# Optimization experiments

Measured on AMD Instinct MI355X. Metric: run time of the kernel, lower is better.

Reference implementation:

```python
import jax, jax.numpy as jnp
import numpy as np

B, C, H, W = 4, 32, 64, 64
D_STATE, D_CONV = 16, 4


def _mamba(x, Win, convw, convb, Wx, Wdt, dtb, Alog, D, Wout, dt_rank):
    Bsz, L, _ = x.shape
    d_in, K = convw.shape
    xz = x @ Win.T                                  # (B, L, 2*d_inner)
    xc, z = xz[..., :d_in], xz[..., d_in:]
    xp = jnp.pad(xc, ((0, 0), (K - 1, 0), (0, 0)))  # causal left pad
    xconv = convb + sum(convw[:, k] * xp[:, k:k + L, :] for k in range(K))
    xa = jax.nn.silu(xconv)                         # (B, L, d_inner)
    xdbl = xa @ Wx.T                                # (B, L, dt_rank + 2*N)
    dt = jax.nn.softplus(xdbl[..., :dt_rank] @ Wdt.T + dtb)     # (B, L, d_inner)
    Bm = xdbl[..., dt_rank:dt_rank + D_STATE]                   # (B, L, N)
    Cm = xdbl[..., dt_rank + D_STATE:]                          # (B, L, N)
    A = -jnp.exp(Alog)                                          # (d_inner, N)
    dA = jnp.exp(dt[..., None] * A)                             # (B, L, d_inner, N)
    dBu = dt[..., None] * Bm[:, :, None, :] * xa[..., None]     # (B, L, d_inner, N)

    def step(h, inp):
        dA_t, dBu_t, C_t = inp
        h = dA_t * h + dBu_t
        return h, jnp.einsum('bdn,bn->bd', h, C_t)

    h0 = jnp.zeros((Bsz, d_in, D_STATE), x.dtype)
    _, ys = jax.lax.scan(step, h0, (dA.transpose(1, 0, 2, 3), dBu.transpose(1, 0, 2, 3), Cm.transpose(1, 0, 2)))
    y = ys.transpose(1, 0, 2) + D * xa
    return (y * jax.nn.silu(z)) @ Wout.T


def _line_seqs(x):
    # x: (B,C,H,W) -> four (B, H*W, C) directional scan orders
    hf = x.reshape(B, C, H * W).transpose(0, 2, 1)
    hb = hf[:, ::-1, :]
    wf = x.transpose(0, 1, 3, 2).reshape(B, C, H * W).transpose(0, 2, 1)
    wb = wf[:, ::-1, :]
    return hf, hb, wf, wb


def _oss(fo1, fo2, p1, p2):
    hf, hb, wf, wb = _line_seqs(fo1)
    fop = jnp.concatenate([hf, hb, wf, wb], axis=2)       # (B, HW, 4C)
    fop = _mamba(fop, *p1, dt_rank=8)
    fop = fop.reshape(B, H * W, 4, C).sum(2)              # (B, HW, C)
    fop = fop.transpose(0, 2, 1).reshape(B, C, H, W)
    residual = fop * fo2
    foc = residual.mean(axis=(2, 3)).reshape(B, C, 1)     # adaptive_avg_pool2d (1,1)
    foc = jnp.concatenate([foc, foc[:, ::-1, :]], axis=2) # (B, C, 2)
    foc = _mamba(foc, *p2, dt_rank=1)
    foc = foc.sum(2, keepdims=True)[..., None]            # (B, C, 1, 1)
    return foc * residual + residual


def setup_inputs() -> dict:
    key = jax.random.key(0)
    ks = jax.random.split(key, 18)
    def n(k, shape, s=0.02):
        return jax.random.normal(k, shape, jnp.float32) * s
    dm1, di1, dr1 = 4 * C, 8 * C, 8
    dm2, di2, dr2 = 2, 4, 1
    return {
        'fo1': jax.random.normal(ks[0], (B, C, H, W), jnp.float32),
        'fo2': jax.random.normal(ks[1], (B, C, H, W), jnp.float32),
        'm1_Win': n(ks[2], (2 * di1, dm1)),
        'm1_convw': n(ks[3], (di1, D_CONV), 0.2),
        'm1_convb': n(ks[4], (di1,), 0.1),
        'm1_Wx': n(ks[5], (dr1 + 2 * D_STATE, di1)),
        'm1_Wdt': n(ks[6], (di1, dr1), 0.1),
        'm1_dtb': n(ks[7], (di1,), 0.5),
        'm1_Alog': jnp.log(jnp.tile(jnp.arange(1, D_STATE + 1, dtype=jnp.float32), (di1, 1))),
        'm1_D': jnp.ones((di1,), jnp.float32),
        'm1_Wout': n(ks[8], (dm1, di1)),
        'm2_Win': n(ks[9], (2 * di2, dm2)),
        'm2_convw': n(ks[10], (di2, D_CONV), 0.2),
        'm2_convb': n(ks[11], (di2,), 0.1),
        'm2_Wx': n(ks[12], (dr2 + 2 * D_STATE, di2)),
        'm2_Wdt': n(ks[13], (di2, dr2), 0.1),
        'm2_dtb': n(ks[14], (di2,), 0.5),
        'm2_Alog': jnp.log(jnp.tile(jnp.arange(1, D_STATE + 1, dtype=jnp.float32), (di2, 1))),
        'm2_D': jnp.ones((di2,), jnp.float32),
        'm2_Wout': n(ks[15], (dm2, di2)),
    }


def reference(fo1, fo2, m1_Win, m1_convw, m1_convb, m1_Wx, m1_Wdt, m1_dtb, m1_Alog, m1_D, m1_Wout,
              m2_Win, m2_convw, m2_convb, m2_Wx, m2_Wdt, m2_dtb, m2_Alog, m2_D, m2_Wout):
    p1 = (m1_Win, m1_convw, m1_convb, m1_Wx, m1_Wdt, m1_dtb, m1_Alog, m1_D, m1_Wout)
    p2 = (m2_Win, m2_convw, m2_convb, m2_Wx, m2_Wdt, m2_dtb, m2_Alog, m2_D, m2_Wout)
    return _oss(fo1, fo2, p1, p2)
```

## Files before the change

### kernel.cpp

```cpp
#include <hip/hip_runtime.h>
#include <cstddef>


typedef __attribute__((ext_vector_type(8))) short short8v;
typedef __attribute__((ext_vector_type(4))) float f32x4;

__device__ __forceinline__ float siluf(float x) { return x / (1.f + __expf(-x)); }
__device__ __forceinline__ float softplusf(float x) { return (x > 20.f) ? x : log1pf(__expf(x)); }
__device__ __forceinline__ unsigned short f2bf(float f) {
  union { float f; unsigned int u; } v; v.f = f;
  unsigned int r = v.u + 0x7fff + ((v.u >> 16) & 1);
  return (unsigned short)(r >> 16);
}

__global__ __launch_bounds__(256) void k_build_fop(const float* __restrict__ fo1,
                                                   unsigned short* __restrict__ fopb) {
  int idx = blockIdx.x * 256 + threadIdx.x;
  int j = idx & 127;
  int l = (idx >> 7) & 4095;
  int b = idx >> 19;
  int g = j >> 5, c = j & 31;
  const float* base = fo1 + (size_t)(b * 32 + c) * 4096;
  int li;
  if (g == 0)      li = l;
  else if (g == 1) li = 4095 - l;
  else if (g == 2) li = ((l & 63) << 6) + (l >> 6);
  else { int i2 = 4095 - l; li = ((i2 & 63) << 6) + (i2 >> 6); }
  fopb[idx] = f2bf(base[li]);
}

__global__ __launch_bounds__(256) void k_gemm1_mfma(const unsigned short* __restrict__ A,
                                                    const float* __restrict__ Win,
                                                    float* __restrict__ C) {
  __shared__ unsigned short As[128][136];
  __shared__ unsigned short Bs[64][136];
  int t = threadIdx.x;
  int bm = blockIdx.x * 128, bn = blockIdx.y * 64;
#pragma unroll
  for (int it = 0; it < 8; ++it) {
    int idx = t + it * 256;
    int r = idx >> 4, kc = idx & 15;
    short8v v = *(const short8v*)&A[(size_t)(bm + r) * 128 + kc * 8];
    *(short8v*)&As[r][kc * 8] = v;
  }
#pragma unroll
  for (int it = 0; it < 8; ++it) {
    int idx = t + it * 256;
    int r = idx >> 5, kq = idx & 31;
    float4 w = *(const float4*)&Win[(size_t)(bn + r) * 128 + kq * 4];
    ushort4 h;
    h.x = f2bf(w.x); h.y = f2bf(w.y); h.z = f2bf(w.z); h.w = f2bf(w.w);
    *(ushort4*)&Bs[r][kq * 4] = h;
  }
  __syncthreads();
  int lane = t & 63, w = t >> 6;
  int wm = (w & 1) * 64, wn = (w >> 1) * 32;
  int lr = lane & 15, lg = lane >> 4;
  f32x4 acc[4][2] = {};
#pragma unroll
  for (int k0 = 0; k0 < 128; k0 += 32) {
    short8v a[4], b[2];
#pragma unroll
    for (int mf = 0; mf < 4; ++mf)
      a[mf] = *(const short8v*)&As[wm + mf * 16 + lr][k0 + lg * 8];
#pragma unroll
    for (int nf = 0; nf < 2; ++nf)
      b[nf] = *(const short8v*)&Bs[wn + nf * 16 + lr][k0 + lg * 8];
#pragma unroll
    for (int mf = 0; mf < 4; ++mf)
#pragma unroll
      for (int nf = 0; nf < 2; ++nf)
        acc[mf][nf] = __builtin_amdgcn_mfma_f32_16x16x32_bf16(a[mf], b[nf], acc[mf][nf], 0, 0, 0);
  }
#pragma unroll
  for (int mf = 0; mf < 4; ++mf)
#pragma unroll
    for (int nf = 0; nf < 2; ++nf)
#pragma unroll
      for (int r = 0; r < 4; ++r) {
        size_t row = bm + wm + mf * 16 + lg * 4 + r;
        C[row * 512 + bn + wn + nf * 16 + lr] = acc[mf][nf][r];
      }
}

__global__ __launch_bounds__(256) void k_gemm_nt(const float* __restrict__ A,
                                                 const float* __restrict__ W,
                                                 float* __restrict__ C,
                                                 int M, int N, int K, int lda) {
  __shared__ float As[32][68];
  __shared__ float Ws[32][68];
  int tid = threadIdx.x;
  int bm = blockIdx.x * 64;
  int bn = blockIdx.y * 64;
  int tx = tid & 15, ty = tid >> 4;
  float acc[4][4] = {};
  for (int k0 = 0; k0 < K; k0 += 32) {
#pragma unroll
    for (int it = 0; it < 2; ++it) {
      int idx = tid + it * 256;
      int r = idx >> 3;
      int kq = idx & 7;
      float4 v = *(const float4*)&A[(size_t)(bm + r) * lda + k0 + kq * 4];
      As[kq * 4 + 0][r] = v.x; As[kq * 4 + 1][r] = v.y;
      As[kq * 4 + 2][r] = v.z; As[kq * 4 + 3][r] = v.w;
      int n = bn + r;
      float4 w = make_float4(0.f, 0.f, 0.f, 0.f);
      if (n < N) w = *(const float4*)&W[(size_t)n * K + k0 + kq * 4];
      Ws[kq * 4 + 0][r] = w.x; Ws[kq * 4 + 1][r] = w.y;
      Ws[kq * 4 + 2][r] = w.z; Ws[kq * 4 + 3][r] = w.w;
    }
    __syncthreads();
#pragma unroll
    for (int k = 0; k < 32; ++k) {
      float4 a = *(const float4*)&As[k][ty * 4];
      float4 w = *(const float4*)&Ws[k][tx * 4];
      float av[4] = {a.x, a.y, a.z, a.w};
      float wv[4] = {w.x, w.y, w.z, w.w};
#pragma unroll
      for (int i = 0; i < 4; ++i)
#pragma unroll
        for (int j = 0; j < 4; ++j)
          acc[i][j] = fmaf(av[i], wv[j], acc[i][j]);
    }
    __syncthreads();
  }
#pragma unroll
  for (int i = 0; i < 4; ++i) {
    size_t m = bm + ty * 4 + i;
#pragma unroll
    for (int j = 0; j < 4; ++j) {
      int n = bn + tx * 4 + j;
      if (n < N) C[m * N + n] = acc[i][j];
    }
  }
}

__global__ __launch_bounds__(256) void k_conv_silu(const float* __restrict__ xz,
                                                   const float* __restrict__ convw,
                                                   const float* __restrict__ convb,
                                                   float* __restrict__ xa) {
  int row = blockIdx.x;
  int l = row & 4095;
  int d = threadIdx.x;
  float4 w = *(const float4*)&convw[d * 4];
  float acc = convb[d];
  const float* p = xz + (size_t)row * 512 + d;
  if (l >= 3) acc = fmaf(w.x, p[-3 * 512], acc);
  if (l >= 2) acc = fmaf(w.y, p[-2 * 512], acc);
  if (l >= 1) acc = fmaf(w.z, p[-1 * 512], acc);
  acc = fmaf(w.w, p[0], acc);
  xa[(size_t)row * 256 + d] = siluf(acc);
}

__global__ __launch_bounds__(256) void k_scan_p1(const float* __restrict__ xa,
                                                 const float* __restrict__ xdbl,
                                                 const float* __restrict__ Wdt,
                                                 const float* __restrict__ dtb,
                                                 const float* __restrict__ Alog,
                                                 float* __restrict__ Pb,
                                                 float* __restrict__ Qb) {
  __shared__ f32x4 xrow[32][10];
  __shared__ float xas[32][256];
  int t = threadIdx.x;
  int blk = blockIdx.x;
  int ch = blk & 127, b = blk >> 7;
  size_t row0 = (size_t)b * 4096 + ch * 32;
  for (int i = t; i < 320; i += 256) {
    int s = i / 10, q = i - s * 10;
    xrow[s][q] = *(const f32x4*)&xdbl[(row0 + s) * 40 + q * 4];
  }
#pragma unroll
  for (int it = 0; it < 8; ++it) {
    int i = t + it * 256;
    int s = i >> 6, q = i & 63;
    *(f32x4*)&xas[s][q * 4] = *(const f32x4*)&xa[(row0 + s) * 256 + q * 4];
  }
  __syncthreads();
  int d = t;
  f32x4 w0 = *(const f32x4*)&Wdt[d * 8];
  f32x4 w1 = *(const f32x4*)&Wdt[d * 8 + 4];
  float bias = dtb[d];
  float A[16], P[16], Q[16];
#pragma unroll
  for (int g = 0; g < 4; ++g) {
    f32x4 al = *(const f32x4*)&Alog[d * 16 + g * 4];
#pragma unroll
    for (int j = 0; j < 4; ++j) {
      A[g * 4 + j] = -__expf(al[j]);
      P[g * 4 + j] = 1.f;
      Q[g * 4 + j] = 0.f;
    }
  }
#pragma unroll 2
  for (int s = 0; s < 32; ++s) {
    f32x4 x0 = xrow[s][0], x1 = xrow[s][1];
    float v = bias;
#pragma unroll
    for (int j = 0; j < 4; ++j) v = fmaf(x0[j], w0[j], v);
#pragma unroll
    for (int j = 0; j < 4; ++j) v = fmaf(x1[j], w1[j], v);
    float ex = __expf(v);
    float dtv = (v > 20.f) ? v : __logf(1.f + ex);
    float du = dtv * xas[s][d];
    f32x4 bm[4];
#pragma unroll
    for (int g = 0; g < 4; ++g) bm[g] = xrow[s][2 + g];
#pragma unroll
    for (int n = 0; n < 16; ++n) {
      float e = __expf(dtv * A[n]);
      Q[n] = fmaf(e, Q[n], du * bm[n >> 2][n & 3]);
      P[n] *= e;
    }
  }
  size_t ob = (size_t)ch * 16384 + b * 4096 + d * 16;
#pragma unroll
  for (int g = 0; g < 4; ++g) {
    *(f32x4*)&Pb[ob + g * 4] = *(f32x4*)&P[g * 4];
    *(f32x4*)&Qb[ob + g * 4] = *(f32x4*)&Q[g * 4];
  }
}

__global__ __launch_bounds__(256) void k_scan_p2(const float* __restrict__ Pb,
                                                 const float* __restrict__ Qb,
                                                 float* __restrict__ Hin) {
  int t = blockIdx.x * 256 + threadIdx.x;
  float h = 0.f;
  size_t o = t;
#pragma unroll 8
  for (int ch = 0; ch < 128; ++ch) {
    Hin[o] = h;
    h = fmaf(Pb[o], h, Qb[o]);
    o += 16384;
  }
}

__global__ __launch_bounds__(256) void k_scan_p3(const float* __restrict__ xa,
                                                 const float* __restrict__ xdbl,
                                                 const float* __restrict__ Wdt,
                                                 const float* __restrict__ dtb,
                                                 const float* __restrict__ Alog,
                                                 const float* __restrict__ Hin,
                                                 const float* __restrict__ Dp,
                                                 const float* __restrict__ xz,
                                                 float* __restrict__ ym) {
  __shared__ f32x4 xrow[32][10];
  __shared__ float xas[32][256];
  int t = threadIdx.x;
  int blk = blockIdx.x;
  int ch = blk & 127, b = blk >> 7;
  size_t row0 = (size_t)b * 4096 + ch * 32;
  for (int i = t; i < 320; i += 256) {
    int s = i / 10, q = i - s * 10;
    xrow[s][q] = *(const f32x4*)&xdbl[(row0 + s) * 40 + q * 4];
  }
#pragma unroll
  for (int it = 0; it < 8; ++it) {
    int i = t + it * 256;
    int s = i >> 6, q = i & 63;
    *(f32x4*)&xas[s][q * 4] = *(const f32x4*)&xa[(row0 + s) * 256 + q * 4];
  }
  __syncthreads();
  int d = t;
  f32x4 w0 = *(const f32x4*)&Wdt[d * 8];
  f32x4 w1 = *(const f32x4*)&Wdt[d * 8 + 4];
  float bias = dtb[d];
  float Dd = Dp[d];
  float A[16], h[16];
  size_t hb = (size_t)ch * 16384 + b * 4096 + d * 16;
#pragma unroll
  for (int g = 0; g < 4; ++g) {
    f32x4 al = *(const f32x4*)&Alog[d * 16 + g * 4];
    f32x4 hv = *(const f32x4*)&Hin[hb + g * 4];
#pragma unroll
    for (int j = 0; j < 4; ++j) {
      A[g * 4 + j] = -__expf(al[j]);
      h[g * 4 + j] = hv[j];
    }
  }
  const float* zp = xz + row0 * 512 + 256 + d;
  float* yo = ym + row0 * 256 + d;
#pragma unroll 2
  for (int s = 0; s < 32; ++s) {
    f32x4 x0 = xrow[s][0], x1 = xrow[s][1];
    float v = bias;
#pragma unroll
    for (int j = 0; j < 4; ++j) v = fmaf(x0[j], w0[j], v);
#pragma unroll
    for (int j = 0; j < 4; ++j) v = fmaf(x1[j], w1[j], v);
    float ex = __expf(v);
    float dtv = (v > 20.f) ? v : __logf(1.f + ex);
    float xav = xas[s][d];
    float du = dtv * xav;
    f32x4 bm[4], cm[4];
#pragma unroll
    for (int g = 0; g < 4; ++g) { bm[g] = xrow[s][2 + g]; cm[g] = xrow[s][6 + g]; }
    float y0 = 0.f, y1 = 0.f, y2 = 0.f, y3 = 0.f;
#pragma unroll
    for (int n = 0; n < 16; n += 4) {
      float e0 = __expf(dtv * A[n]);
      float e1 = __expf(dtv * A[n + 1]);
      float e2 = __expf(dtv * A[n + 2]);
      float e3 = __expf(dtv * A[n + 3]);
      f32x4 bv = bm[n >> 2], cv = cm[n >> 2];
      h[n]     = fmaf(e0, h[n],     du * bv[0]);
      h[n + 1] = fmaf(e1, h[n + 1], du * bv[1]);
      h[n + 2] = fmaf(e2, h[n + 2], du * bv[2]);
      h[n + 3] = fmaf(e3, h[n + 3], du * bv[3]);
      y0 = fmaf(h[n], cv[0], y0);
      y1 = fmaf(h[n + 1], cv[1], y1);
      y2 = fmaf(h[n + 2], cv[2], y2);
      y3 = fmaf(h[n + 3], cv[3], y3);
    }
    float y = (y0 + y1) + (y2 + y3) + Dd * xav;
    float z = zp[s * 512];
    yo[s * 256] = y * siluf(z);
  }
}

__global__ __launch_bounds__(256) void k_gemm3(const float* __restrict__ A,
                                               const float* __restrict__ Wout,
                                               float* __restrict__ CT) {
  __shared__ float As[32][68];
  __shared__ float Ws[32][68];
  int tid = threadIdx.x;
  int bm = blockIdx.x * 64;
  int tx = tid & 15, ty = tid >> 4;
  float acc[4][4] = {};
  for (int k0 = 0; k0 < 256; k0 += 32) {
#pragma unroll
    for (int it = 0; it < 2; ++it) {
      int idx = tid + it * 256;
      int r = idx >> 3;
      int kq = idx & 7;
      float4 v = *(const float4*)&A[(size_t)(bm + r) * 256 + k0 + kq * 4];
      As[kq * 4 + 0][r] = v.x; As[kq * 4 + 1][r] = v.y;
      As[kq * 4 + 2][r] = v.z; As[kq * 4 + 3][r] = v.w;
      float4 w = make_float4(0.f, 0.f, 0.f, 0.f);
      if (r < 32) {
#pragma unroll
        for (int g = 0; g < 4; ++g) {
          float4 wg = *(const float4*)&Wout[(size_t)(r + g * 32) * 256 + k0 + kq * 4];
          w.x += wg.x; w.y += wg.y; w.z += wg.z; w.w += wg.w;
        }
      }
      Ws[kq * 4 + 0][r] = w.x; Ws[kq * 4 + 1][r] = w.y;
      Ws[kq * 4 + 2][r] = w.z; Ws[kq * 4 + 3][r] = w.w;
    }
    __syncthreads();
#pragma unroll
    for (int k = 0; k < 32; ++k) {
      float4 a = *(const float4*)&As[k][ty * 4];
      float4 w = *(const float4*)&Ws[k][tx * 4];
      float av[4] = {a.x, a.y, a.z, a.w};
      float wv[4] = {w.x, w.y, w.z, w.w};
#pragma unroll
      for (int i = 0; i < 4; ++i)
#pragma unroll
        for (int j = 0; j < 4; ++j)
          acc[i][j] = fmaf(av[i], wv[j], acc[i][j]);
    }
    __syncthreads();
  }
#pragma unroll
  for (int j = 0; j < 4; ++j) {
    int n = tx * 4 + j;
    if (n < 32) {
      float4 v = make_float4(acc[0][j], acc[1][j], acc[2][j], acc[3][j]);
      *(float4*)&CT[(size_t)n * 16384 + bm + ty * 4] = v;
    }
  }
}

__global__ __launch_bounds__(256) void k_res_foc(const float* __restrict__ CT,
                                                 const float* __restrict__ fo2,
                                                 float* __restrict__ res,
                                                 float* __restrict__ foc) {
  int bc = blockIdx.x;
  int b = bc >> 5, c = bc & 31;
  int t = threadIdx.x;
  const float* src = CT + (size_t)c * 16384 + (size_t)b * 4096;
  const float* f2 = fo2 + (size_t)bc * 4096;
  float* rp = res + (size_t)bc * 4096;
  float s = 0.f;
  for (int i = t * 4; i < 4096; i += 1024) {
    float4 a = *(const float4*)&src[i];
    float4 f = *(const float4*)&f2[i];
    float4 r = make_float4(a.x * f.x, a.y * f.y, a.z * f.z, a.w * f.w);
    *(float4*)&rp[i] = r;
    s += r.x + r.y + r.z + r.w;
  }
  __shared__ float red[256];
  red[t] = s;
  __syncthreads();
  for (int off = 128; off > 0; off >>= 1) {
    if (t < off) red[t] += red[t + off];
    __syncthreads();
  }
  if (t == 0) foc[bc] = red[0] * (1.f / 4096.f);
}

__global__ __launch_bounds__(256) void k_mamba2(const float* __restrict__ foc,
                                                const float* __restrict__ Win2,
                                                const float* __restrict__ convw2,
                                                const float* __restrict__ convb2,
                                                const float* __restrict__ Wx2,
                                                const float* __restrict__ Wdt2,
                                                const float* __restrict__ dtb2,
                                                const float* __restrict__ Alog2,
                                                const float* __restrict__ D2,
                                                const float* __restrict__ Wout2,
                                                float* __restrict__ scale) {
  __shared__ float foc_s[128];
  __shared__ float xz2_s[4][32][8];
  __shared__ float xa2_s[4][32][4];
  __shared__ float xdbl2_s[4][32][33];
  __shared__ float dt2_s[4][32][4];
  __shared__ float ym2_s[4][32][4];
  int t = threadIdx.x;
  if (t < 128) foc_s[t] = foc[t];
  __syncthreads();
  for (int i = t; i < 1024; i += 256) {
    int j = i & 7, l = (i >> 3) & 31, b = i >> 8;
    float x0 = foc_s[b * 32 + l], x1 = foc_s[b * 32 + 31 - l];
    xz2_s[b][l][j] = x0 * Win2[j * 2] + x1 * Win2[j * 2 + 1];
  }
  __syncthreads();
  for (int i = t; i < 512; i += 256) {
    int d = i & 3, l = (i >> 2) & 31, b = i >> 7;
    float acc = convb2[d];
#pragma unroll
    for (int k = 0; k < 4; ++k) {
      int ls = l + k - 3;
      if (ls >= 0) acc = fmaf(convw2[d * 4 + k], xz2_s[b][ls][d], acc);
    }
    xa2_s[b][l][d] = siluf(acc);
  }
  __syncthreads();
  for (int i = t; i < 4224; i += 256) {
    int r = i % 33, l = (i / 33) & 31, b = i / 1056;
    float s = 0.f;
#pragma unroll
    for (int d = 0; d < 4; ++d) s = fmaf(xa2_s[b][l][d], Wx2[r * 4 + d], s);
    xdbl2_s[b][l][r] = s;
  }
  __syncthreads();
  for (int i = t; i < 512; i += 256) {
    int d = i & 3, l = (i >> 2) & 31, b = i >> 7;
    float s = xdbl2_s[b][l][0] * Wdt2[d] + dtb2[d];
    dt2_s[b][l][d] = softplusf(s);
  }
  __syncthreads();
  {
    int n = t & 15, d = (t >> 4) & 3, b = t >> 6;
    float A = -__expf(Alog2[d * 16 + n]);
    float h = 0.f;
    for (int l = 0; l < 32; ++l) {
      float dtv = dt2_s[b][l][d];
      float xav = xa2_s[b][l][d];
      float e = __expf(dtv * A);
      h = fmaf(e, h, dtv * xdbl2_s[b][l][1 + n] * xav);
      float yp = h * xdbl2_s[b][l][17 + n];
      yp += __shfl_xor(yp, 1);
      yp += __shfl_xor(yp, 2);
      yp += __shfl_xor(yp, 4);
      yp += __shfl_xor(yp, 8);
      if (n == 0) {
        float z = xz2_s[b][l][4 + d];
        float y = yp + D2[d] * xav;
        ym2_s[b][l][d] = y * siluf(z);
      }
    }
  }
  __syncthreads();
  if (t < 128) {
    int l = t & 31, b = t >> 5;
    float s = 0.f;
#pragma unroll
    for (int d = 0; d < 4; ++d) s = fmaf(ym2_s[b][l][d], Wout2[d] + Wout2[4 + d], s);
    scale[t] = s;
  }
}

__global__ __launch_bounds__(256) void k_final(const float* __restrict__ res,
                                               const float* __restrict__ scale,
                                               float* __restrict__ out) {
  int idx = blockIdx.x * 256 + threadIdx.x;
  out[idx] = res[idx] * (1.f + scale[idx >> 12]);
}

extern "C" void kernel_launch(void* const* d_in, const int* in_sizes, int n_in,
                              void* d_out, int out_size, void* d_ws, size_t ws_size,
                              hipStream_t stream) {
  const float* fo1    = (const float*)d_in[0];
  const float* fo2    = (const float*)d_in[1];
  const float* Win    = (const float*)d_in[2];
  const float* convw  = (const float*)d_in[3];
  const float* convb  = (const float*)d_in[4];
  const float* Wx     = (const float*)d_in[5];
  const float* Wdt    = (const float*)d_in[6];
  const float* dtb    = (const float*)d_in[7];
  const float* Alog   = (const float*)d_in[8];
  const float* Dp     = (const float*)d_in[9];
  const float* Wout   = (const float*)d_in[10];
  const float* Win2   = (const float*)d_in[11];
  const float* convw2 = (const float*)d_in[12];
  const float* convb2 = (const float*)d_in[13];
  const float* Wx2    = (const float*)d_in[14];
  const float* Wdt2   = (const float*)d_in[15];
  const float* dtb2   = (const float*)d_in[16];
  const float* Alog2  = (const float*)d_in[17];
  const float* D2     = (const float*)d_in[18];
  const float* Wout2  = (const float*)d_in[19];

  float* ws = (float*)d_ws;
  unsigned short* fopb = (unsigned short*)ws;
  float* xdbl = ws;
  float* xz   = ws + 1048576;
  float* xa   = ws + 9437184;
  float* Pb   = ws + 13631488;
  float* Qb   = ws + 15728640;
  float* Hin  = ws + 17825792;
  float* ym   = ws + 19922944;
  float* o1T  = ws + 24117248;
  float* res  = ws + 24641536;
  float* foc  = ws + 25165824;
  float* scl  = ws + 25165952;
  if (ws_size < (size_t)25166080 * sizeof(float)) return;

  hipLaunchKernelGGL(k_build_fop, dim3(8192), dim3(256), 0, stream, fo1, fopb);
  hipLaunchKernelGGL(k_gemm1_mfma, dim3(128, 8), dim3(256), 0, stream, fopb, Win, xz);
  hipLaunchKernelGGL(k_conv_silu, dim3(16384), dim3(256), 0, stream, xz, convw, convb, xa);
  hipLaunchKernelGGL(k_gemm_nt, dim3(256, 1), dim3(256), 0, stream,
                     xa, Wx, xdbl, 16384, 40, 256, 256);
  hipLaunchKernelGGL(k_scan_p1, dim3(512), dim3(256), 0, stream,
                     xa, xdbl, Wdt, dtb, Alog, Pb, Qb);
  hipLaunchKernelGGL(k_scan_p2, dim3(64), dim3(256), 0, stream, Pb, Qb, Hin);
  hipLaunchKernelGGL(k_scan_p3, dim3(512), dim3(256), 0, stream,
                     xa, xdbl, Wdt, dtb, Alog, Hin, Dp, xz, ym);
  hipLaunchKernelGGL(k_gemm3, dim3(256), dim3(256), 0, stream, ym, Wout, o1T);
  hipLaunchKernelGGL(k_res_foc, dim3(128), dim3(256), 0, stream, o1T, fo2, res, foc);
  hipLaunchKernelGGL(k_mamba2, dim3(1), dim3(256), 0, stream, foc, Win2, convw2, convb2,
                     Wx2, Wdt2, dtb2, Alog2, D2, Wout2, scl);
  hipLaunchKernelGGL(k_final, dim3(2048), dim3(256), 0, stream, res, scl, (float*)d_out);
}
```

Baseline: 156.0 us.

## Fuse conv/silu/x-proj into scan pass, bf16 MFMA out-proj fused with residual

Conv+SiLU and the x-projection GEMM move into a new front kernel that also runs the first scan pass, so the xa tensor is never written. The third scan pass recomputes conv+SiLU from xz and writes ym as bf16. The output projection now uses bf16 MFMA and fuses the fo2 multiply and per-block partial means, which k_mamba2 then reduces. This removes several launches and large intermediate round-trips, at the cost of redundant conv work, extra shared memory per block (lower occupancy) and bf16 rounding of ym and Wout.

```diff
diff --git a/kernel.cpp b/kernel.cpp
--- a/kernel.cpp
+++ b/kernel.cpp
@@ -83,140 +83,123 @@
       }
 }
 
-__global__ __launch_bounds__(256) void k_gemm_nt(const float* __restrict__ A,
-                                                 const float* __restrict__ W,
-                                                 float* __restrict__ C,
-                                                 int M, int N, int K, int lda) {
-  __shared__ float As[32][68];
-  __shared__ float Ws[32][68];
-  int tid = threadIdx.x;
-  int bm = blockIdx.x * 64;
-  int bn = blockIdx.y * 64;
-  int tx = tid & 15, ty = tid >> 4;
-  float acc[4][4] = {};
-  for (int k0 = 0; k0 < K; k0 += 32) {
-#pragma unroll
-    for (int it = 0; it < 2; ++it) {
-      int idx = tid + it * 256;
-      int r = idx >> 3;
-      int kq = idx & 7;
-      float4 v = *(const float4*)&A[(size_t)(bm + r) * lda + k0 + kq * 4];
-      As[kq * 4 + 0][r] = v.x; As[kq * 4 + 1][r] = v.y;
-      As[kq * 4 + 2][r] = v.z; As[kq * 4 + 3][r] = v.w;
-      int n = bn + r;
-      float4 w = make_float4(0.f, 0.f, 0.f, 0.f);
-      if (n < N) w = *(const float4*)&W[(size_t)n * K + k0 + kq * 4];
-      Ws[kq * 4 + 0][r] = w.x; Ws[kq * 4 + 1][r] = w.y;
-      Ws[kq * 4 + 2][r] = w.z; Ws[kq * 4 + 3][r] = w.w;
-    }
-    __syncthreads();
-#pragma unroll
-    for (int k = 0; k < 32; ++k) {
-      float4 a = *(const float4*)&As[k][ty * 4];
-      float4 w = *(const float4*)&Ws[k][tx * 4];
-      float av[4] = {a.x, a.y, a.z, a.w};
-      float wv[4] = {w.x, w.y, w.z, w.w};
-#pragma unroll
-      for (int i = 0; i < 4; ++i)
-#pragma unroll
-        for (int j = 0; j < 4; ++j)
-          acc[i][j] = fmaf(av[i], wv[j], acc[i][j]);
-    }
-    __syncthreads();
-  }
-#pragma unroll
-  for (int i = 0; i < 4; ++i) {
-    size_t m = bm + ty * 4 + i;
-#pragma unroll
-    for (int j = 0; j < 4; ++j) {
-      int n = bn + tx * 4 + j;
-      if (n < N) C[m * N + n] = acc[i][j];
-    }
-  }
-}
-
-__global__ __launch_bounds__(256) void k_conv_silu(const float* __restrict__ xz,
-                                                   const float* __restrict__ convw,
-                                                   const float* __restrict__ convb,
-                                                   float* __restrict__ xa) {
-  int row = blockIdx.x;
-  int l = row & 4095;
-  int d = threadIdx.x;
-  float4 w = *(const float4*)&convw[d * 4];
-  float acc = convb[d];
-  const float* p = xz + (size_t)row * 512 + d;
-  if (l >= 3) acc = fmaf(w.x, p[-3 * 512], acc);
-  if (l >= 2) acc = fmaf(w.y, p[-2 * 512], acc);
-  if (l >= 1) acc = fmaf(w.z, p[-1 * 512], acc);
-  acc = fmaf(w.w, p[0], acc);
-  xa[(size_t)row * 256 + d] = siluf(acc);
-}
-
-__global__ __launch_bounds__(256) void k_scan_p1(const float* __restrict__ xa,
-                                                 const float* __restrict__ xdbl,
-                                                 const float* __restrict__ Wdt,
-                                                 const float* __restrict__ dtb,
-                                                 const float* __restrict__ Alog,
-                                                 float* __restrict__ Pb,
-                                                 float* __restrict__ Qb) {
-  __shared__ f32x4 xrow[32][10];
-  __shared__ float xas[32][256];
+__global__ __launch_bounds__(256) void k_front(const float* __restrict__ xz,
+                                               const float* __restrict__ convw,
+                                               const float* __restrict__ convb,
+                                               const float* __restrict__ Wx,
+                                               const float* __restrict__ Wdt,
+                                               const float* __restrict__ dtb,
+                                               const float* __restrict__ Alog,
+                                               float* __restrict__ xdbl_g,
+                                               float* __restrict__ Pb,
+                                               float* __restrict__ Qb) {
+  __shared__ float bufU[10400];
+  __shared__ float xas[32][260];
+  __shared__ float xdbl_s[32][40];
   int t = threadIdx.x;
   int blk = blockIdx.x;
   int ch = blk & 127, b = blk >> 7;
   size_t row0 = (size_t)b * 4096 + ch * 32;
-  for (int i = t; i < 320; i += 256) {
-    int s = i / 10, q = i - s * 10;
-    xrow[s][q] = *(const f32x4*)&xdbl[(row0 + s) * 40 + q * 4];
-  }
-#pragma unroll
-  for (int it = 0; it < 8; ++it) {
-    int i = t + it * 256;
-    int s = i >> 6, q = i & 63;
-    *(f32x4*)&xas[s][q * 4] = *(const f32x4*)&xa[(row0 + s) * 256 + q * 4];
-  }
-  __syncthreads();
-  int d = t;
-  f32x4 w0 = *(const f32x4*)&Wdt[d * 8];
-  f32x4 w1 = *(const f32x4*)&Wdt[d * 8 + 4];
-  float bias = dtb[d];
-  float A[16], P[16], Q[16];
-#pragma unroll
-  for (int g = 0; g < 4; ++g) {
-    f32x4 al = *(const f32x4*)&Alog[d * 16 + g * 4];
-#pragma unroll
-    for (int j = 0; j < 4; ++j) {
-      A[g * 4 + j] = -__expf(al[j]);
-      P[g * 4 + j] = 1.f;
-      Q[g * 4 + j] = 0.f;
-    }
-  }
+
+  for (int i = t; i < 8960; i += 256) {
+    int rr = i >> 8, c = i & 255;
+    float v = 0.f;
+    if (ch > 0 || rr >= 3) v = xz[(row0 - 3 + rr) * 512 + c];
+    bufU[rr * 260 + c] = v;
+  }
+  __syncthreads();
+  {
+    int s = t >> 3, dg = t & 7;
+#pragma unroll 8
+    for (int j = 0; j < 32; ++j) {
+      int d = dg + 8 * j;
+      float4 w = *(const float4*)&convw[d * 4];
+      float acc = convb[d];
+      acc = fmaf(w.x, bufU[(s + 0) * 260 + d], acc);
+      acc = fmaf(w.y, bufU[(s + 1) * 260 + d], acc);
+      acc = fmaf(w.z, bufU[(s + 2) * 260 + d], acc);
+      acc = fmaf(w.w, bufU[(s + 3) * 260 + d], acc);
+      xas[s][d] = siluf(acc);
+    }
+  }
+  __syncthreads();
+  for (int i = t; i < 10400; i += 256) {
+    int r = i / 260, c = i - r * 260;
+    bufU[i] = (c < 256) ? Wx[r * 256 + c] : 0.f;
+  }
+  __syncthreads();
+  {
+    int s = t >> 3, tg = t & 7;
+    float a0 = 0.f, a1 = 0.f, a2 = 0.f, a3 = 0.f, a4 = 0.f;
+    for (int d4 = 0; d4 < 64; ++d4) {
+      f32x4 xv = *(const f32x4*)&xas[s][d4 * 4];
+      f32x4 w0 = *(const f32x4*)&bufU[(tg) * 260 + d4 * 4];
+      f32x4 w1 = *(const f32x4*)&bufU[(tg + 8) * 260 + d4 * 4];
+      f32x4 w2 = *(const f32x4*)&bufU[(tg + 16) * 260 + d4 * 4];
+      f32x4 w3 = *(const f32x4*)&bufU[(tg + 24) * 260 + d4 * 4];
+      f32x4 w4 = *(const f32x4*)&bufU[(tg + 32) * 260 + d4 * 4];
+#pragma unroll
+      for (int j = 0; j < 4; ++j) {
+        a0 = fmaf(xv[j], w0[j], a0);
+        a1 = fmaf(xv[j], w1[j], a1);
+        a2 = fmaf(xv[j], w2[j], a2);
+        a3 = fmaf(xv[j], w3[j], a3);
+        a4 = fmaf(xv[j], w4[j], a4);
+      }
+    }
+    xdbl_s[s][tg]      = a0;
+    xdbl_s[s][tg + 8]  = a1;
+    xdbl_s[s][tg + 16] = a2;
+    xdbl_s[s][tg + 24] = a3;
+    xdbl_s[s][tg + 32] = a4;
+  }
+  __syncthreads();
+  for (int i = t; i < 1280; i += 256)
+    xdbl_g[row0 * 40 + i] = ((const float*)xdbl_s)[i];
+  {
+    int d = t;
+    f32x4 w0 = *(const f32x4*)&Wdt[d * 8];
+    f32x4 w1 = *(const f32x4*)&Wdt[d * 8 + 4];
+    float bias = dtb[d];
+    float A[16], P[16], Q[16];
+#pragma unroll
+    for (int g = 0; g < 4; ++g) {
+      f32x4 al = *(const f32x4*)&Alog[d * 16 + g * 4];
+#pragma unroll
+      for (int j = 0; j < 4; ++j) {
+        A[g * 4 + j] = -__expf(al[j]);
+        P[g * 4 + j] = 1.f;
+        Q[g * 4 + j] = 0.f;
+      }
+    }
 #pragma unroll 2
-  for (int s = 0; s < 32; ++s) {
-    f32x4 x0 = xrow[s][0], x1 = xrow[s][1];
-    float v = bias;
-#pragma unroll
-    for (int j = 0; j < 4; ++j) v = fmaf(x0[j], w0[j], v);
-#pragma unroll
-    for (int j = 0; j < 4; ++j) v = fmaf(x1[j], w1[j], v);
-    float ex = __expf(v);
-    float dtv = (v > 20.f) ? v : __logf(1.f + ex);
-    float du = dtv * xas[s][d];
-    f32x4 bm[4];
-#pragma unroll
-    for (int g = 0; g < 4; ++g) bm[g] = xrow[s][2 + g];
-#pragma unroll
-    for (int n = 0; n < 16; ++n) {
-      float e = __expf(dtv * A[n]);
-      Q[n] = fmaf(e, Q[n], du * bm[n >> 2][n & 3]);
-      P[n] *= e;
-    }
-  }
-  size_t ob = (size_t)ch * 16384 + b * 4096 + d * 16;
-#pragma unroll
-  for (int g = 0; g < 4; ++g) {
-    *(f32x4*)&Pb[ob + g * 4] = *(f32x4*)&P[g * 4];
-    *(f32x4*)&Qb[ob + g * 4] = *(f32x4*)&Q[g * 4];
+    for (int s = 0; s < 32; ++s) {
+      f32x4 x0 = *(const f32x4*)&xdbl_s[s][0];
+      f32x4 x1 = *(const f32x4*)&xdbl_s[s][4];
+      float v = bias;
+#pragma unroll
+      for (int j = 0; j < 4; ++j) v = fmaf(x0[j], w0[j], v);
+#pragma unroll
+      for (int j = 0; j < 4; ++j) v = fmaf(x1[j], w1[j], v);
+      float ex = __expf(v);
+      float dtv = (v > 20.f) ? v : __logf(1.f + ex);
+      float du = dtv * xas[s][d];
+      f32x4 bm[4];
+#pragma unroll
+      for (int g = 0; g < 4; ++g) bm[g] = *(const f32x4*)&xdbl_s[s][8 + g * 4];
+#pragma unroll
+      for (int n = 0; n < 16; ++n) {
+        float e = __expf(dtv * A[n]);
+        Q[n] = fmaf(e, Q[n], du * bm[n >> 2][n & 3]);
+        P[n] *= e;
+      }
+    }
+    size_t ob = (size_t)ch * 16384 + b * 4096 + d * 16;
+#pragma unroll
+    for (int g = 0; g < 4; ++g) {
+      *(f32x4*)&Pb[ob + g * 4] = *(f32x4*)&P[g * 4];
+      *(f32x4*)&Qb[ob + g * 4] = *(f32x4*)&Q[g * 4];
+    }
   }
 }
 
@@ -234,30 +217,45 @@
   }
 }
 
-__global__ __launch_bounds__(256) void k_scan_p3(const float* __restrict__ xa,
-                                                 const float* __restrict__ xdbl,
+__global__ __launch_bounds__(256) void k_scan_p3(const float* __restrict__ xz,
+                                                 const float* __restrict__ convw,
+                                                 const float* __restrict__ convb,
+                                                 const float* __restrict__ xdbl_g,
                                                  const float* __restrict__ Wdt,
                                                  const float* __restrict__ dtb,
                                                  const float* __restrict__ Alog,
                                                  const float* __restrict__ Hin,
                                                  const float* __restrict__ Dp,
-                                                 const float* __restrict__ xz,
-                                                 float* __restrict__ ym) {
-  __shared__ f32x4 xrow[32][10];
-  __shared__ float xas[32][256];
+                                                 unsigned short* __restrict__ ym) {
+  __shared__ float xcs[9100];
+  __shared__ float xas[32][260];
+  __shared__ float xrow[1280];
   int t = threadIdx.x;
   int blk = blockIdx.x;
   int ch = blk & 127, b = blk >> 7;
   size_t row0 = (size_t)b * 4096 + ch * 32;
-  for (int i = t; i < 320; i += 256) {
-    int s = i / 10, q = i - s * 10;
-    xrow[s][q] = *(const f32x4*)&xdbl[(row0 + s) * 40 + q * 4];
-  }
-#pragma unroll
-  for (int it = 0; it < 8; ++it) {
-    int i = t + it * 256;
-    int s = i >> 6, q = i & 63;
-    *(f32x4*)&xas[s][q * 4] = *(const f32x4*)&xa[(row0 + s) * 256 + q * 4];
+
+  for (int i = t; i < 8960; i += 256) {
+    int rr = i >> 8, c = i & 255;
+    float v = 0.f;
+    if (ch > 0 || rr >= 3) v = xz[(row0 - 3 + rr) * 512 + c];
+    xcs[rr * 260 + c] = v;
+  }
+  for (int i = t; i < 1280; i += 256) xrow[i] = xdbl_g[row0 * 40 + i];
+  __syncthreads();
+  {
+    int s = t >> 3, dg = t & 7;
+#pragma unroll 8
+    for (int j = 0; j < 32; ++j) {
+      int d = dg + 8 * j;
+      float4 w = *(const float4*)&convw[d * 4];
+      float acc = convb[d];
+      acc = fmaf(w.x, xcs[(s + 0) * 260 + d], acc);
+      acc = fmaf(w.y, xcs[(s + 1) * 260 + d], acc);
+      acc = fmaf(w.z, xcs[(s + 2) * 260 + d], acc);
+      acc = fmaf(w.w, xcs[(s + 3) * 260 + d], acc);
+      xas[s][d] = siluf(acc);
+    }
   }
   __syncthreads();
   int d = t;
@@ -278,10 +276,11 @@
     }
   }
   const float* zp = xz + row0 * 512 + 256 + d;
-  float* yo = ym + row0 * 256 + d;
+  unsigned short* yo = ym + row0 * 256 + d;
 #pragma unroll 2
   for (int s = 0; s < 32; ++s) {
-    f32x4 x0 = xrow[s][0], x1 = xrow[s][1];
+    f32x4 x0 = *(const f32x4*)&xrow[s * 40];
+    f32x4 x1 = *(const f32x4*)&xrow[s * 40 + 4];
     float v = bias;
 #pragma unroll
     for (int j = 0; j < 4; ++j) v = fmaf(x0[j], w0[j], v);
@@ -291,17 +290,15 @@
     float dtv = (v > 20.f) ? v : __logf(1.f + ex);
     float xav = xas[s][d];
     float du = dtv * xav;
-    f32x4 bm[4], cm[4];
-#pragma unroll
-    for (int g = 0; g < 4; ++g) { bm[g] = xrow[s][2 + g]; cm[g] = xrow[s][6 + g]; }
     float y0 = 0.f, y1 = 0.f, y2 = 0.f, y3 = 0.f;
 #pragma unroll
     for (int n = 0; n < 16; n += 4) {
+      f32x4 bv = *(const f32x4*)&xrow[s * 40 + 8 + n];
+      f32x4 cv = *(const f32x4*)&xrow[s * 40 + 24 + n];
       float e0 = __expf(dtv * A[n]);
       float e1 = __expf(dtv * A[n + 1]);
       float e2 = __expf(dtv * A[n + 2]);
       float e3 = __expf(dtv * A[n + 3]);
-      f32x4 bv = bm[n >> 2], cv = cm[n >> 2];
       h[n]     = fmaf(e0, h[n],     du * bv[0]);
       h[n + 1] = fmaf(e1, h[n + 1], du * bv[1]);
       h[n + 2] = fmaf(e2, h[n + 2], du * bv[2]);
@@ -313,93 +310,68 @@
     }
     float y = (y0 + y1) + (y2 + y3) + Dd * xav;
     float z = zp[s * 512];
-    yo[s * 256] = y * siluf(z);
-  }
-}
-
-__global__ __launch_bounds__(256) void k_gemm3(const float* __restrict__ A,
-                                               const float* __restrict__ Wout,
-                                               float* __restrict__ CT) {
-  __shared__ float As[32][68];
-  __shared__ float Ws[32][68];
-  int tid = threadIdx.x;
+    yo[s * 256] = f2bf(y * siluf(z));
+  }
+}
+
+__global__ __launch_bounds__(256) void k_gemm3res(const unsigned short* __restrict__ ym,
+                                                  const float* __restrict__ Wout,
+                                                  const float* __restrict__ fo2,
+                                                  float* __restrict__ res,
+                                                  float* __restrict__ focp) {
+  __shared__ unsigned short As[64][264];
+  __shared__ unsigned short Bs[32][264];
+  __shared__ float fred[4][32];
+  int t = threadIdx.x;
   int bm = blockIdx.x * 64;
-  int tx = tid & 15, ty = tid >> 4;
-  float acc[4][4] = {};
+#pragma unroll
+  for (int it = 0; it < 8; ++it) {
+    int idx = t + it * 256;
+    int r = idx >> 5, kc = idx & 31;
+    *(short8v*)&As[r][kc * 8] = *(const short8v*)&ym[(size_t)(bm + r) * 256 + kc * 8];
+  }
+#pragma unroll
+  for (int it = 0; it < 32; ++it) {
+    int idx = t + it * 256;
+    int n = idx >> 8, k = idx & 255;
+    float wv = Wout[(size_t)n * 256 + k] + Wout[(size_t)(n + 32) * 256 + k] +
+               Wout[(size_t)(n + 64) * 256 + k] + Wout[(size_t)(n + 96) * 256 + k];
+    Bs[n][k] = f2bf(wv);
+  }
+  __syncthreads();
+  int lane = t & 63, w = t >> 6;
+  int lr = lane & 15, lg = lane >> 4;
+  f32x4 acc0 = {}, acc1 = {};
+#pragma unroll
   for (int k0 = 0; k0 < 256; k0 += 32) {
-#pragma unroll
-    for (int it = 0; it < 2; ++it) {
-      int idx = tid + it * 256;
-      int r = idx >> 3;
-      int kq = idx & 7;
-      float4 v = *(const float4*)&A[(size_t)(bm + r) * 256 + k0 + kq * 4];
-      As[kq * 4 + 0][r] = v.x; As[kq * 4 + 1][r] = v.y;
-      As[kq * 4 + 2][r] = v.z; As[kq * 4 + 3][r] = v.w;
-      float4 w = make_float4(0.f, 0.f, 0.f, 0.f);
-      if (r < 32) {
-#pragma unroll
-        for (int g = 0; g < 4; ++g) {
-          float4 wg = *(const float4*)&Wout[(size_t)(r + g * 32) * 256 + k0 + kq * 4];
-          w.x += wg.x; w.y += wg.y; w.z += wg.z; w.w += wg.w;
-        }
-      }
-      Ws[kq * 4 + 0][r] = w.x; Ws[kq * 4 + 1][r] = w.y;
-      Ws[kq * 4 + 2][r] = w.z; Ws[kq * 4 + 3][r] = w.w;
-    }
-    __syncthreads();
-#pragma unroll
-    for (int k = 0; k < 32; ++k) {
-      float4 a = *(const float4*)&As[k][ty * 4];
-      float4 w = *(const float4*)&Ws[k][tx * 4];
-      float av[4] = {a.x, a.y, a.z, a.w};
-      float wv[4] = {w.x, w.y, w.z, w.w};
-#pragma unroll
-      for (int i = 0; i < 4; ++i)
-#pragma unroll
-        for (int j = 0; j < 4; ++j)
-          acc[i][j] = fmaf(av[i], wv[j], acc[i][j]);
-    }
-    __syncthreads();
-  }
-#pragma unroll
-  for (int j = 0; j < 4; ++j) {
-    int n = tx * 4 + j;
-    if (n < 32) {
-      float4 v = make_float4(acc[0][j], acc[1][j], acc[2][j], acc[3][j]);
-      *(float4*)&CT[(size_t)n * 16384 + bm + ty * 4] = v;
-    }
-  }
-}
-
-__global__ __launch_bounds__(256) void k_res_foc(const float* __restrict__ CT,
-                                                 const float* __restrict__ fo2,
-                                                 float* __restrict__ res,
-                                                 float* __restrict__ foc) {
-  int bc = blockIdx.x;
-  int b = bc >> 5, c = bc & 31;
-  int t = threadIdx.x;
-  const float* src = CT + (size_t)c * 16384 + (size_t)b * 4096;
-  const float* f2 = fo2 + (size_t)bc * 4096;
-  float* rp = res + (size_t)bc * 4096;
-  float s = 0.f;
-  for (int i = t * 4; i < 4096; i += 1024) {
-    float4 a = *(const float4*)&src[i];
-    float4 f = *(const float4*)&f2[i];
-    float4 r = make_float4(a.x * f.x, a.y * f.y, a.z * f.z, a.w * f.w);
-    *(float4*)&rp[i] = r;
-    s += r.x + r.y + r.z + r.w;
-  }
-  __shared__ float red[256];
-  red[t] = s;
-  __syncthreads();
-  for (int off = 128; off > 0; off >>= 1) {
-    if (t < off) red[t] += red[t + off];
-    __syncthreads();
-  }
-  if (t == 0) foc[bc] = red[0] * (1.f / 4096.f);
-}
-
-__global__ __launch_bounds__(256) void k_mamba2(const float* __restrict__ foc,
+    short8v a  = *(const short8v*)&As[w * 16 + lr][k0 + lg * 8];
+    short8v b0 = *(const short8v*)&Bs[lr][k0 + lg * 8];
+    short8v b1 = *(const short8v*)&Bs[16 + lr][k0 + lg * 8];
+    acc0 = __builtin_amdgcn_mfma_f32_16x16x32_bf16(a, b0, acc0, 0, 0, 0);
+    acc1 = __builtin_amdgcn_mfma_f32_16x16x32_bf16(a, b1, acc1, 0, 0, 0);
+  }
+  int b = bm >> 12;
+  float ps0 = 0.f, ps1 = 0.f;
+#pragma unroll
+  for (int r = 0; r < 4; ++r) {
+    int l = (bm + w * 16 + lg * 4 + r) & 4095;
+    size_t ri0 = ((size_t)(b * 32 + lr)) * 4096 + l;
+    size_t ri1 = ((size_t)(b * 32 + 16 + lr)) * 4096 + l;
+    float v0 = acc0[r] * fo2[ri0];
+    float v1 = acc1[r] * fo2[ri1];
+    res[ri0] = v0; ps0 += v0;
+    res[ri1] = v1; ps1 += v1;
+  }
+  ps0 += __shfl_xor(ps0, 16); ps0 += __shfl_xor(ps0, 32);
+  ps1 += __shfl_xor(ps1, 16); ps1 += __shfl_xor(ps1, 32);
+  if (lane < 16) { fred[w][lane] = ps0; fred[w][16 + lane] = ps1; }
+  __syncthreads();
+  if (t < 32)
+    focp[((size_t)(b * 32 + t)) * 64 + (blockIdx.x & 63)] =
+        fred[0][t] + fred[1][t] + fred[2][t] + fred[3][t];
+}
+
+__global__ __launch_bounds__(256) void k_mamba2(const float* __restrict__ focp,
                                                 const float* __restrict__ Win2,
                                                 const float* __restrict__ convw2,
                                                 const float* __restrict__ convb2,
@@ -417,7 +389,11 @@
   __shared__ float dt2_s[4][32][4];
   __shared__ float ym2_s[4][32][4];
   int t = threadIdx.x;
-  if (t < 128) foc_s[t] = foc[t];
+  if (t < 128) {
+    float s = 0.f;
+    for (int k = 0; k < 64; ++k) s += focp[(size_t)t * 64 + k];
+    foc_s[t] = s * (1.f / 4096.f);
+  }
   __syncthreads();
   for (int i = t; i < 1024; i += 256) {
     int j = i & 7, l = (i >> 3) & 31, b = i >> 8;
@@ -516,30 +492,24 @@
   unsigned short* fopb = (unsigned short*)ws;
   float* xdbl = ws;
   float* xz   = ws + 1048576;
-  float* xa   = ws + 9437184;
-  float* Pb   = ws + 13631488;
-  float* Qb   = ws + 15728640;
-  float* Hin  = ws + 17825792;
-  float* ym   = ws + 19922944;
-  float* o1T  = ws + 24117248;
-  float* res  = ws + 24641536;
-  float* foc  = ws + 25165824;
-  float* scl  = ws + 25165952;
-  if (ws_size < (size_t)25166080 * sizeof(float)) return;
+  float* Pb   = ws + 9437184;
+  float* Qb   = ws + 11534336;
+  float* Hin  = ws + 13631488;
+  unsigned short* ym = (unsigned short*)(ws + 15728640);
+  float* res  = ws + 17825792;
+  float* focp = ws + 18350080;
+  float* scl  = ws + 18358272;
+  if (ws_size < (size_t)18358400 * sizeof(float)) return;
 
   hipLaunchKernelGGL(k_build_fop, dim3(8192), dim3(256), 0, stream, fo1, fopb);
   hipLaunchKernelGGL(k_gemm1_mfma, dim3(128, 8), dim3(256), 0, stream, fopb, Win, xz);
-  hipLaunchKernelGGL(k_conv_silu, dim3(16384), dim3(256), 0, stream, xz, convw, convb, xa);
-  hipLaunchKernelGGL(k_gemm_nt, dim3(256, 1), dim3(256), 0, stream,
-                     xa, Wx, xdbl, 16384, 40, 256, 256);
-  hipLaunchKernelGGL(k_scan_p1, dim3(512), dim3(256), 0, stream,
-                     xa, xdbl, Wdt, dtb, Alog, Pb, Qb);
+  hipLaunchKernelGGL(k_front, dim3(512), dim3(256), 0, stream,
+                     xz, convw, convb, Wx, Wdt, dtb, Alog, xdbl, Pb, Qb);
   hipLaunchKernelGGL(k_scan_p2, dim3(64), dim3(256), 0, stream, Pb, Qb, Hin);
   hipLaunchKernelGGL(k_scan_p3, dim3(512), dim3(256), 0, stream,
-                     xa, xdbl, Wdt, dtb, Alog, Hin, Dp, xz, ym);
-  hipLaunchKernelGGL(k_gemm3, dim3(256), dim3(256), 0, stream, ym, Wout, o1T);
-  hipLaunchKernelGGL(k_res_foc, dim3(128), dim3(256), 0, stream, o1T, fo2, res, foc);
-  hipLaunchKernelGGL(k_mamba2, dim3(1), dim3(256), 0, stream, foc, Win2, convw2, convb2,
+                     xz, convw, convb, xdbl, Wdt, dtb, Alog, Hin, Dp, ym);
+  hipLaunchKernelGGL(k_gemm3res, dim3(256), dim3(256), 0, stream, ym, Wout, fo2, res, focp);
+  hipLaunchKernelGGL(k_mamba2, dim3(1), dim3(256), 0, stream, focp, Win2, convw2, convb2,
                      Wx2, Wdt2, dtb2, Alog2, D2, Wout2, scl);
   hipLaunchKernelGGL(k_final, dim3(2048), dim3(256), 0, stream, res, scl, (float*)d_out);
 }
```

Result: faster. 146.7 us (-6.0%).

## Fuse output GEMM with residual multiply and pooling using bf16 MFMA

Applied to the files above, without the earlier changes.

The scan kernel now writes its gated output in bf16. A new kernel replaces the fp32 FMA output GEMM and the separate residual/pool kernel. It uses MFMA bf16 16x16x32, multiplies by fo2 in the epilogue, and writes per-block partial channel sums that the second mamba kernel reduces. This removes the o1T intermediate round trip and one launch, and halves ym traffic. The cost is bf16 rounding of activations and weights, plus uncoalesced strided res/fo2 accesses in the epilogue.

```diff
diff --git a/kernel.cpp b/kernel.cpp
--- a/kernel.cpp
+++ b/kernel.cpp
@@ -242,7 +242,7 @@
                                                  const float* __restrict__ Hin,
                                                  const float* __restrict__ Dp,
                                                  const float* __restrict__ xz,
-                                                 float* __restrict__ ym) {
+                                                 unsigned short* __restrict__ ym) {
   __shared__ f32x4 xrow[32][10];
   __shared__ float xas[32][256];
   int t = threadIdx.x;
@@ -278,7 +278,7 @@
     }
   }
   const float* zp = xz + row0 * 512 + 256 + d;
-  float* yo = ym + row0 * 256 + d;
+  unsigned short* yo = ym + row0 * 256 + d;
 #pragma unroll 2
   for (int s = 0; s < 32; ++s) {
     f32x4 x0 = xrow[s][0], x1 = xrow[s][1];
@@ -313,93 +313,68 @@
     }
     float y = (y0 + y1) + (y2 + y3) + Dd * xav;
     float z = zp[s * 512];
-    yo[s * 256] = y * siluf(z);
-  }
-}
-
-__global__ __launch_bounds__(256) void k_gemm3(const float* __restrict__ A,
-                                               const float* __restrict__ Wout,
-                                               float* __restrict__ CT) {
-  __shared__ float As[32][68];
-  __shared__ float Ws[32][68];
-  int tid = threadIdx.x;
+    yo[s * 256] = f2bf(y * siluf(z));
+  }
+}
+
+__global__ __launch_bounds__(256) void k_gemm3res(const unsigned short* __restrict__ ym,
+                                                  const float* __restrict__ Wout,
+                                                  const float* __restrict__ fo2,
+                                                  float* __restrict__ res,
+                                                  float* __restrict__ focp) {
+  __shared__ unsigned short As[64][264];
+  __shared__ unsigned short Bs[32][264];
+  __shared__ float fred[4][32];
+  int t = threadIdx.x;
   int bm = blockIdx.x * 64;
-  int tx = tid & 15, ty = tid >> 4;
-  float acc[4][4] = {};
+#pragma unroll
+  for (int it = 0; it < 8; ++it) {
+    int idx = t + it * 256;
+    int r = idx >> 5, kc = idx & 31;
+    *(short8v*)&As[r][kc * 8] = *(const short8v*)&ym[(size_t)(bm + r) * 256 + kc * 8];
+  }
+#pragma unroll
+  for (int it = 0; it < 32; ++it) {
+    int idx = t + it * 256;
+    int n = idx >> 8, k = idx & 255;
+    float wv = Wout[(size_t)n * 256 + k] + Wout[(size_t)(n + 32) * 256 + k] +
+               Wout[(size_t)(n + 64) * 256 + k] + Wout[(size_t)(n + 96) * 256 + k];
+    Bs[n][k] = f2bf(wv);
+  }
+  __syncthreads();
+  int lane = t & 63, w = t >> 6;
+  int lr = lane & 15, lg = lane >> 4;
+  f32x4 acc0 = {}, acc1 = {};
+#pragma unroll
   for (int k0 = 0; k0 < 256; k0 += 32) {
-#pragma unroll
-    for (int it = 0; it < 2; ++it) {
-      int idx = tid + it * 256;
-      int r = idx >> 3;
-      int kq = idx & 7;
-      float4 v = *(const float4*)&A[(size_t)(bm + r) * 256 + k0 + kq * 4];
-      As[kq * 4 + 0][r] = v.x; As[kq * 4 + 1][r] = v.y;
-      As[kq * 4 + 2][r] = v.z; As[kq * 4 + 3][r] = v.w;
-      float4 w = make_float4(0.f, 0.f, 0.f, 0.f);
-      if (r < 32) {
-#pragma unroll
-        for (int g = 0; g < 4; ++g) {
-          float4 wg = *(const float4*)&Wout[(size_t)(r + g * 32) * 256 + k0 + kq * 4];
-          w.x += wg.x; w.y += wg.y; w.z += wg.z; w.w += wg.w;
-        }
-      }
-      Ws[kq * 4 + 0][r] = w.x; Ws[kq * 4 + 1][r] = w.y;
-      Ws[kq * 4 + 2][r] = w.z; Ws[kq * 4 + 3][r] = w.w;
-    }
-    __syncthreads();
-#pragma unroll
-    for (int k = 0; k < 32; ++k) {
-      float4 a = *(const float4*)&As[k][ty * 4];
-      float4 w = *(const float4*)&Ws[k][tx * 4];
-      float av[4] = {a.x, a.y, a.z, a.w};
-      float wv[4] = {w.x, w.y, w.z, w.w};
-#pragma unroll
-      for (int i = 0; i < 4; ++i)
-#pragma unroll
-        for (int j = 0; j < 4; ++j)
-          acc[i][j] = fmaf(av[i], wv[j], acc[i][j]);
-    }
-    __syncthreads();
-  }
-#pragma unroll
-  for (int j = 0; j < 4; ++j) {
-    int n = tx * 4 + j;
-    if (n < 32) {
-      float4 v = make_float4(acc[0][j], acc[1][j], acc[2][j], acc[3][j]);
-      *(float4*)&CT[(size_t)n * 16384 + bm + ty * 4] = v;
-    }
-  }
-}
-
-__global__ __launch_bounds__(256) void k_res_foc(const float* __restrict__ CT,
-                                                 const float* __restrict__ fo2,
-                                                 float* __restrict__ res,
-                                                 float* __restrict__ foc) {
-  int bc = blockIdx.x;
-  int b = bc >> 5, c = bc & 31;
-  int t = threadIdx.x;
-  const float* src = CT + (size_t)c * 16384 + (size_t)b * 4096;
-  const float* f2 = fo2 + (size_t)bc * 4096;
-  float* rp = res + (size_t)bc * 4096;
-  float s = 0.f;
-  for (int i = t * 4; i < 4096; i += 1024) {
-    float4 a = *(const float4*)&src[i];
-    float4 f = *(const float4*)&f2[i];
-    float4 r = make_float4(a.x * f.x, a.y * f.y, a.z * f.z, a.w * f.w);
-    *(float4*)&rp[i] = r;
-    s += r.x + r.y + r.z + r.w;
-  }
-  __shared__ float red[256];
-  red[t] = s;
-  __syncthreads();
-  for (int off = 128; off > 0; off >>= 1) {
-    if (t < off) red[t] += red[t + off];
-    __syncthreads();
-  }
-  if (t == 0) foc[bc] = red[0] * (1.f / 4096.f);
-}
-
-__global__ __launch_bounds__(256) void k_mamba2(const float* __restrict__ foc,
+    short8v a  = *(const short8v*)&As[w * 16 + lr][k0 + lg * 8];
+    short8v b0 = *(const short8v*)&Bs[lr][k0 + lg * 8];
+    short8v b1 = *(const short8v*)&Bs[16 + lr][k0 + lg * 8];
+    acc0 = __builtin_amdgcn_mfma_f32_16x16x32_bf16(a, b0, acc0, 0, 0, 0);
+    acc1 = __builtin_amdgcn_mfma_f32_16x16x32_bf16(a, b1, acc1, 0, 0, 0);
+  }
+  int b = bm >> 12;
+  float ps0 = 0.f, ps1 = 0.f;
+#pragma unroll
+  for (int r = 0; r < 4; ++r) {
+    int l = (bm + w * 16 + lg * 4 + r) & 4095;
+    size_t ri0 = ((size_t)(b * 32 + lr)) * 4096 + l;
+    size_t ri1 = ((size_t)(b * 32 + 16 + lr)) * 4096 + l;
+    float v0 = acc0[r] * fo2[ri0];
+    float v1 = acc1[r] * fo2[ri1];
+    res[ri0] = v0; ps0 += v0;
+    res[ri1] = v1; ps1 += v1;
+  }
+  ps0 += __shfl_xor(ps0, 16); ps0 += __shfl_xor(ps0, 32);
+  ps1 += __shfl_xor(ps1, 16); ps1 += __shfl_xor(ps1, 32);
+  if (lane < 16) { fred[w][lane] = ps0; fred[w][16 + lane] = ps1; }
+  __syncthreads();
+  if (t < 32)
+    focp[((size_t)(b * 32 + t)) * 64 + (blockIdx.x & 63)] =
+        fred[0][t] + fred[1][t] + fred[2][t] + fred[3][t];
+}
+
+__global__ __launch_bounds__(256) void k_mamba2(const float* __restrict__ focp,
                                                 const float* __restrict__ Win2,
                                                 const float* __restrict__ convw2,
                                                 const float* __restrict__ convb2,
@@ -417,7 +392,11 @@
   __shared__ float dt2_s[4][32][4];
   __shared__ float ym2_s[4][32][4];
   int t = threadIdx.x;
-  if (t < 128) foc_s[t] = foc[t];
+  if (t < 128) {
+    float s = 0.f;
+    for (int k = 0; k < 64; ++k) s += focp[(size_t)t * 64 + k];
+    foc_s[t] = s * (1.f / 4096.f);
+  }
   __syncthreads();
   for (int i = t; i < 1024; i += 256) {
     int j = i & 7, l = (i >> 3) & 31, b = i >> 8;
@@ -520,12 +499,11 @@
   float* Pb   = ws + 13631488;
   float* Qb   = ws + 15728640;
   float* Hin  = ws + 17825792;
-  float* ym   = ws + 19922944;
-  float* o1T  = ws + 24117248;
-  float* res  = ws + 24641536;
-  float* foc  = ws + 25165824;
-  float* scl  = ws + 25165952;
-  if (ws_size < (size_t)25166080 * sizeof(float)) return;
+  unsigned short* ym = (unsigned short*)(ws + 19922944);
+  float* res  = ws + 22020096;
+  float* focp = ws + 22544384;
+  float* scl  = ws + 22552576;
+  if (ws_size < (size_t)22552704 * sizeof(float)) return;
 
   hipLaunchKernelGGL(k_build_fop, dim3(8192), dim3(256), 0, stream, fo1, fopb);
   hipLaunchKernelGGL(k_gemm1_mfma, dim3(128, 8), dim3(256), 0, stream, fopb, Win, xz);
@@ -537,9 +515,8 @@
   hipLaunchKernelGGL(k_scan_p2, dim3(64), dim3(256), 0, stream, Pb, Qb, Hin);
   hipLaunchKernelGGL(k_scan_p3, dim3(512), dim3(256), 0, stream,
                      xa, xdbl, Wdt, dtb, Alog, Hin, Dp, xz, ym);
-  hipLaunchKernelGGL(k_gemm3, dim3(256), dim3(256), 0, stream, ym, Wout, o1T);
-  hipLaunchKernelGGL(k_res_foc, dim3(128), dim3(256), 0, stream, o1T, fo2, res, foc);
-  hipLaunchKernelGGL(k_mamba2, dim3(1), dim3(256), 0, stream, foc, Win2, convw2, convb2,
+  hipLaunchKernelGGL(k_gemm3res, dim3(256), dim3(256), 0, stream, ym, Wout, fo2, res, focp);
+  hipLaunchKernelGGL(k_mamba2, dim3(1), dim3(256), 0, stream, focp, Win2, convw2, convb2,
                      Wx2, Wdt2, dtb2, Alog2, D2, Wout2, scl);
   hipLaunchKernelGGL(k_final, dim3(2048), dim3(256), 0, stream, res, scl, (float*)d_out);
 }
```

After: 140.5 us. 10.0% less time.
